# Kernel optimization log

Hardware: AMD Instinct MI355X
Metric: run time of the kernel (lower is better)

## Reference

```python
import jax, jax.numpy as jnp
import numpy as np

NH, HD = 8, 32  # num_heads, head_dim (visual_dim=256)
BASE = 10000.0

def _inv_freq(dim):
    return 1.0 / (BASE ** (jnp.arange(0, dim, 2, dtype=jnp.float32) / dim))

def rotate_half(x):
    x1, x2 = jnp.split(x, 2, axis=-1)
    return jnp.concatenate([-x2, x1], axis=-1)

def rope3d_freqs(D, H, W, head_dim):
    zd = head_dim // 3; yd = head_dim // 3; xd = head_dim - zd - yd
    fz = jnp.arange(D, dtype=jnp.float32)[:, None] * _inv_freq(zd)  # [D, zd/2]
    fy = jnp.arange(H, dtype=jnp.float32)[:, None] * _inv_freq(yd)
    fx = jnp.arange(W, dtype=jnp.float32)[:, None] * _inv_freq(xd)
    ez = jnp.broadcast_to(jnp.concatenate([fz, fz], -1)[:, None, None, :], (D, H, W, zd))
    ey = jnp.broadcast_to(jnp.concatenate([fy, fy], -1)[None, :, None, :], (D, H, W, yd))
    ex = jnp.broadcast_to(jnp.concatenate([fx, fx], -1)[None, None, :, :], (D, H, W, xd))
    return jnp.concatenate([ez, ey, ex], axis=-1)  # [D,H,W,head_dim]

def apply_rope(q, freqs):
    return q * jnp.cos(freqs) + rotate_half(q) * jnp.sin(freqs)

def setup_inputs() -> dict:
    key = jax.random.key(0)
    ks = jax.random.split(key, 16)
    B, C, D, H, W, S, TD = 2, 256, 32, 32, 32, 256, 512
    s = 0.02
    return {
        'fused_visual': jax.random.normal(ks[0], (B, C, D, H, W), jnp.float32),
        'text_embedding': jax.random.normal(ks[1], (B, S, TD), jnp.float32),
        'q_w': jax.random.normal(ks[2], (C, C), jnp.float32) * s,
        'q_b': jnp.zeros((C,), jnp.float32),
        'k_w': jax.random.normal(ks[3], (TD, C), jnp.float32) * s,
        'k_b': jnp.zeros((C,), jnp.float32),
        'v_w': jax.random.normal(ks[4], (TD, C), jnp.float32) * s,
        'v_b': jnp.zeros((C,), jnp.float32),
        'o_w': jax.random.normal(ks[5], (C, C), jnp.float32) * s,
        'o_b': jnp.zeros((C,), jnp.float32),
        'm1_w': jax.random.normal(ks[6], (TD, TD // 2), jnp.float32) * s,
        'm1_b': jnp.zeros((TD // 2,), jnp.float32),
        'm2_w': jax.random.normal(ks[7], (TD // 2, NH * HD), jnp.float32) * s,
        'm2_b': jnp.zeros((NH * HD,), jnp.float32),
    }

def reference(fused_visual, text_embedding, q_w, q_b, k_w, k_b, v_w, v_b,
              o_w, o_b, m1_w, m1_b, m2_w, m2_b):
    B, C, D, H, W = fused_visual.shape
    S = text_embedding.shape[1]
    scale = HD ** -0.5
    fv = jnp.transpose(fused_visual, (0, 2, 3, 4, 1))  # [B,D,H,W,C]
    q = (fv @ q_w + q_b).reshape(B, D, H, W, NH, HD)
    q = jnp.transpose(q, (0, 4, 1, 2, 3, 5))            # [B,nH,D,H,W,hd]
    k = jnp.transpose((text_embedding @ k_w + k_b).reshape(B, S, NH, HD), (0, 2, 1, 3))
    v = jnp.transpose((text_embedding @ v_w + v_b).reshape(B, S, NH, HD), (0, 2, 1, 3))
    freqs = rope3d_freqs(D, H, W, HD)[None, None]       # [1,1,D,H,W,hd]
    q_rot = apply_rope(q, freqs)
    # learned text phase (exact GELU as in torch default)
    h = jax.nn.gelu(text_embedding @ m1_w + m1_b, approximate=False)
    phase = jnp.transpose((h @ m2_w + m2_b).reshape(B, S, NH, HD), (0, 2, 1, 3))
    k_rot = apply_rope(k, phase)
    q_flat = q_rot.reshape(B, NH, D * H * W, HD)
    attn = jax.nn.softmax(jnp.einsum('bhnd,bhsd->bhns', q_flat, k_rot) * scale, axis=-1)
    out = jnp.einsum('bhns,bhsd->bhnd', attn, v)        # [B,nH,N,hd]
    out = out.reshape(B, NH, D, H, W, HD)
    out = jnp.transpose(out, (0, 2, 3, 4, 1, 5)).reshape(B, D, H, W, C)
    out = out @ o_w + o_b
    return jnp.transpose(out, (0, 4, 1, 2, 3))          # [B,C,D,H,W]
```

## Files before the change

### kernel.cpp

```cpp
#include <hip/hip_runtime.h>
#include <hip/hip_bf16.h>

#define NHD 8
#define HD  32
#define C_  256
#define TD_ 512
#define S_  256
#define N_  32768
#define B_  2

typedef short bf16x8 __attribute__((ext_vector_type(8)));
typedef short bf16x4 __attribute__((ext_vector_type(4)));
typedef float f32x4  __attribute__((ext_vector_type(4)));

#define MFMA16(a,b,c) __builtin_amdgcn_mfma_f32_16x16x32_bf16(a,b,c,0,0,0)

__device__ __forceinline__ short f2bf(float f){
    __hip_bfloat16 h = __float2bfloat16(f);
    return *reinterpret_cast<short*>(&h);
}

typedef __attribute__((address_space(3))) unsigned int lds_u32;
typedef const __attribute__((address_space(1))) unsigned int glb_u32;

__device__ __forceinline__ void async_cp16(const void* g, void* l){
    __builtin_amdgcn_global_load_lds(
        (glb_u32*)(unsigned long long)g,
        (lds_u32*)(unsigned int)(unsigned long long)l,
        16, 0, 0);
}

__device__ __forceinline__ void stage_tile(const short* __restrict__ g, short* l, int tid){
    const int wvb = tid & 192;
#pragma unroll
    for (int r = 0; r < 4; ++r)
        async_cp16(g + (r * 256 + tid) * 8, l + (r * 256 + wvb) * 8);
}

#define T1_LD(K,V,M,j0) _Pragma("unroll") for(int i=0;i<8;++i){ \
    K[i]=kp[(j0+i)*C_]; V[i]=vp[(j0+i)*C_]; M[i]=mp[(j0+i)*C_]; }
#define T1_FM(K,V,M,j0) _Pragma("unroll") for(int i=0;i<8;++i){ \
    _Pragma("unroll") for(int m=0;m<4;++m){ float tv=t_s[m*TD_+j0+i]; \
        accK[m]+=tv*K[i]; accV[m]+=tv*V[i]; accH[m]+=tv*M[i]; } }

__global__ __launch_bounds__(256) void text1(
    const float* __restrict__ text,
    const float* __restrict__ k_w, const float* __restrict__ k_b,
    const float* __restrict__ v_w, const float* __restrict__ v_b,
    const float* __restrict__ m1_w, const float* __restrict__ m1_b,
    const float* __restrict__ qw, const float* __restrict__ ow,
    float* __restrict__ kraw, float* __restrict__ vraw, float* __restrict__ hgb,
    short* __restrict__ wqf, short* __restrict__ wof)
{
    const int tid = threadIdx.x;

    if (blockIdx.x >= 128) {
        int gid = (blockIdx.x - 128) * 256 + tid;
        int m = gid >> 13;
        int rest = gid & 8191;
        const float* src = m ? ow : qw;
        short* dst = m ? wof : wqf;
        int lane = rest & 63;
        int l15 = lane & 15, qd = lane >> 4;
        int cbase, co;
        if (m == 0) { int nt = rest >> 9, cc = (rest >> 6) & 7; cbase = cc * 32 + qd * 8; co = nt * 16 + l15; }
        else        { int hm = rest >> 6; cbase = (hm >> 4) * 32 + qd * 8; co = (hm & 15) * 16 + l15; }
        bf16x8 r;
#pragma unroll
        for (int j = 0; j < 8; ++j) r[j] = f2bf(src[(size_t)(cbase + j) * 256 + co]);
        *(bf16x8*)&dst[(size_t)rest * 8] = r;
        return;
    }

    __shared__ float t_s[4 * TD_];
    const int tok0 = blockIdx.x * 4;
#pragma unroll
    for (int i = 0; i < 2; ++i) {
        int idx = i * 256 + tid;
        *(float4*)&t_s[idx * 4] = *(const float4*)&text[(size_t)tok0 * TD_ + idx * 4];
    }
    __syncthreads();

    float accK[4], accV[4], accH[4];
#pragma unroll
    for (int m = 0; m < 4; ++m) { accK[m] = k_b[tid]; accV[m] = v_b[tid]; accH[m] = m1_b[tid]; }
    const float* kp = k_w + tid;
    const float* vp = v_w + tid;
    const float* mp = m1_w + tid;

    {
        float ka[8], va[8], ma[8], kb2[8], vb2[8], mb2[8];
        T1_LD(ka, va, ma, 0);
#pragma unroll 1
        for (int j0 = 0; j0 < TD_; j0 += 16) {
            T1_LD(kb2, vb2, mb2, j0 + 8);
            T1_FM(ka, va, ma, j0);
            if (j0 + 16 < TD_) { T1_LD(ka, va, ma, j0 + 16); }
            T1_FM(kb2, vb2, mb2, j0 + 8);
        }
    }

#pragma unroll
    for (int m = 0; m < 4; ++m) {
        kraw[(size_t)(tok0 + m) * C_ + tid] = accK[m];
        vraw[(size_t)(tok0 + m) * C_ + tid] = accV[m];
        float hv = accH[m];
        hgb[(size_t)(tok0 + m) * C_ + tid] = 0.5f * hv * (1.0f + erff(hv * 0.70710678118654752f));
    }
}

#define T2_LD(G, j0) _Pragma("unroll") for (int i = 0; i < 8; ++i) G[i] = m2p[(j0 + i) * C_];
#define T2_FM(G, j0) _Pragma("unroll") for (int i = 0; i < 8; ++i) { \
    _Pragma("unroll") for (int m = 0; m < 8; ++m) accP[m] += h_s[m * C_ + j0 + i] * G[i]; }

__global__ __launch_bounds__(256) void text2(
    const float* __restrict__ m2_w, const float* __restrict__ m2_b,
    const float* __restrict__ kraw, const float* __restrict__ vraw,
    const float* __restrict__ hgb,
    short* __restrict__ kf, short* __restrict__ vf)
{
    __shared__ float h_s[8 * C_];
    const int tid = threadIdx.x;
    const int tok0 = blockIdx.x * 8;
#pragma unroll
    for (int i = 0; i < 2; ++i) {
        int idx = i * 256 + tid;
        *(float4*)&h_s[idx * 4] = *(const float4*)&hgb[(size_t)tok0 * C_ + idx * 4];
    }
    __syncthreads();

    float accP[8];
#pragma unroll
    for (int m = 0; m < 8; ++m) accP[m] = m2_b[tid];
    const float* m2p = m2_w + tid;
    {
        float ga[8], gb2[8];
        T2_LD(ga, 0);
#pragma unroll 1
        for (int j0 = 0; j0 < C_; j0 += 16) {
            T2_LD(gb2, j0 + 8);
            T2_FM(ga, j0);
            if (j0 + 16 < C_) { T2_LD(ga, j0 + 16); }
            T2_FM(gb2, j0 + 8);
        }
    }

    const int t = tid & (HD - 1);
    const int nh = tid >> 5;
#pragma unroll
    for (int m = 0; m < 8; ++m) {
        int token = tok0 + m;
        int b = token >> 8, s = token & (S_ - 1);
        int bh = b * NHD + nh;
        float kv = kraw[(size_t)token * C_ + tid];
        float vv = vraw[(size_t)token * C_ + tid];
        float partner = (t < 16) ? -kraw[(size_t)token * C_ + tid + 16]
                                 :  kraw[(size_t)token * C_ + tid - 16];
        float ph = accP[m];
        float kr = kv * cosf(ph) + partner * sinf(ph);
        kf[(((size_t)bh * 16 + (s >> 4)) * 64 + (t >> 3) * 16 + (s & 15)) * 8 + (t & 7)] = f2bf(kr);
        vf[((((size_t)bh * 8 + (s >> 5)) * 2 + (t >> 4)) * 64 + ((s >> 3) & 3) * 16 + (t & 15)) * 8 + (s & 7)] = f2bf(vv);
    }
}

__device__ __forceinline__ float freq3d(int t, int n){
    int d = n >> 10, h = (n >> 5) & 31, w = n & 31;
    float pos, ex;
    if (t < 10)      { pos = (float)d; ex = (float)(2 * (t % 5)) * 0.1f; }
    else if (t < 20) { pos = (float)h; ex = (float)(2 * ((t - 10) % 5)) * 0.1f; }
    else             { pos = (float)w; ex = (float)(2 * ((t - 20) % 6)) * (1.0f / 12.0f); }
    return pos * expf(-ex * 9.210340371976184f);
}

__global__ __launch_bounds__(256, 4) void fused_visual(
    const float* __restrict__ fv, const short* __restrict__ wqf,
    const float* __restrict__ q_b, const short* __restrict__ kf,
    const short* __restrict__ vf, const short* __restrict__ wof,
    const float* __restrict__ o_b, float* __restrict__ out)
{
    __shared__ __align__(16) short Stg[16384];
    __shared__ __align__(16) short Pb[4 * 16 * 64];
    const int tid = threadIdx.x;
    const int lane = tid & 63;
    const int l15 = tid & 15, qd = (tid >> 4) & 3, wv = tid >> 6;
    const int n0 = blockIdx.x * 64;
    const int b = blockIdx.y;
    const f32x4 z4 = {0.f, 0.f, 0.f, 0.f};
    const float scale = 0.17677669529663687f;

    short* slot0 = Stg;
    short* slot1 = Stg + 8192;

    stage_tile(wqf, slot0, tid);

    bf16x8 af[8];
    {
        const float* fbase = fv + ((size_t)b * C_) * N_ + n0 + wv * 16 + l15;
#pragma unroll
        for (int cc = 0; cc < 8; ++cc) {
            float tmp[8];
#pragma unroll
            for (int j = 0; j < 8; ++j)
                tmp[j] = fbase[(size_t)(cc * 32 + qd * 8 + j) * N_];
#pragma unroll
            for (int j = 0; j < 8; ++j) af[cc][j] = f2bf(tmp[j]);
        }
    }

    f32x4 acc[16];
#pragma unroll
    for (int i = 0; i < 16; ++i) acc[i] = z4;

#pragma unroll
    for (int ntp = 0; ntp < 8; ++ntp) {
        __syncthreads();
        if (ntp < 7) stage_tile(wqf + (ntp + 1) * 8192, (ntp & 1) ? slot0 : slot1, tid);
        const short* sb = (ntp & 1) ? slot1 : slot0;
#pragma unroll
        for (int cc = 0; cc < 8; ++cc)
#pragma unroll
            for (int ntl = 0; ntl < 2; ++ntl) {
                bf16x8 bq = *(const bf16x8*)&sb[((ntl * 8 + cc) * 64 + lane) * 8];
                acc[ntp * 2 + ntl] = MFMA16(af[cc], bq, acc[ntp * 2 + ntl]);
            }
    }
    __syncthreads();

    short* Qsc = Stg + wv * 4096;
#pragma unroll
    for (int r = 0; r < 4; ++r) {
        int lr = qd * 4 + r;
        int n = n0 + wv * 16 + lr;
        int key = lr & 7;
        float f1 = freq3d(l15, n), f2 = freq3d(l15 + 16, n);
        float c1 = cosf(f1), s1 = sinf(f1), c2 = cosf(f2), s2 = sinf(f2);
#pragma unroll
        for (int hh = 0; hh < 8; ++hh) {
            float x1 = acc[2 * hh][r]     + q_b[hh * 32 + l15];
            float x2 = acc[2 * hh + 1][r] + q_b[hh * 32 + 16 + l15];
            int cb1 = (hh * 4 + (l15 >> 3)) ^ key;
            int cb2 = (hh * 4 + 2 + (l15 >> 3)) ^ key;
            Qsc[lr * 256 + cb1 * 8 + (l15 & 7)] = f2bf((x1 * c1 - x2 * s1) * scale);
            Qsc[lr * 256 + cb2 * 8 + (l15 & 7)] = f2bf((x2 * c2 + x1 * s2) * scale);
        }
    }
    bf16x8 aqh[8];
#pragma unroll
    for (int h = 0; h < 8; ++h)
        aqh[h] = *(const bf16x8*)&Qsc[l15 * 256 + ((h * 4 + qd) ^ (l15 & 7)) * 8];

    __syncthreads();
    stage_tile(kf + (size_t)(b * NHD) * 8192, slot0, tid);

    f32x4 acc_co[16];
#pragma unroll
    for (int i = 0; i < 16; ++i) acc_co[i] = z4;
    short* Pw = Pb + wv * 16 * 64;
    short* Ow = Pw;

#pragma unroll
    for (int h = 0; h < 8; ++h) {
        const int bh = b * NHD + h;
        __syncthreads();
        stage_tile(wof + (size_t)h * 8192, slot1, tid);

        const short* vbase = vf + (size_t)bh * 8192;

        float tsum[4] = {0.f, 0.f, 0.f, 0.f};
        f32x4 o0 = z4, o1 = z4;

#pragma unroll
        for (int qt = 0; qt < 4; ++qt) {
            f32x4 sc[4];
#pragma unroll
            for (int s4 = 0; s4 < 4; ++s4) {
                bf16x8 bk = *(const bf16x8*)&slot0[(qt * 4 + s4) * 512 + lane * 8];
                sc[s4] = MFMA16(aqh[h], bk, z4);
            }
#pragma unroll
            for (int s4 = 0; s4 < 4; ++s4)
#pragma unroll
                for (int r = 0; r < 4; ++r) {
                    sc[s4][r] = __expf(sc[s4][r]);
                    tsum[r] += sc[s4][r];
                }
#pragma unroll
            for (int s4 = 0; s4 < 4; ++s4)
#pragma unroll
                for (int r = 0; r < 4; ++r) {
                    int row = qd * 4 + r;
                    Pw[row * 64 + ((s4 * 2 + (l15 >> 3)) ^ (row & 7)) * 8 + (l15 & 7)] = f2bf(sc[s4][r]);
                }
#pragma unroll
            for (int ktl = 0; ktl < 2; ++ktl) {
                bf16x8 pa = *(const bf16x8*)&Pw[l15 * 64 + ((ktl * 4 + qd) ^ (l15 & 7)) * 8];
                int kt = qt * 2 + ktl;
                bf16x8 v0 = *(const bf16x8*)&vbase[(kt * 2 + 0) * 512 + lane * 8];
                bf16x8 v1 = *(const bf16x8*)&vbase[(kt * 2 + 1) * 512 + lane * 8];
                o0 = MFMA16(pa, v0, o0);
                o1 = MFMA16(pa, v1, o1);
            }
        }
        float il[4];
#pragma unroll
        for (int r = 0; r < 4; ++r) {
            float t = tsum[r];
            t += __shfl_xor(t, 1); t += __shfl_xor(t, 2);
            t += __shfl_xor(t, 4); t += __shfl_xor(t, 8);
            il[r] = 1.f / t;
        }
#pragma unroll
        for (int r = 0; r < 4; ++r) {
            int row = qd * 4 + r;
            int key = row & 3;
            Ow[row * 32 + (((l15 >> 3) ^ key) & 3) * 8 + (l15 & 7)]       = f2bf(o0[r] * il[r]);
            Ow[row * 32 + (((2 + (l15 >> 3)) ^ key) & 3) * 8 + (l15 & 7)] = f2bf(o1[r] * il[r]);
        }

        __syncthreads();
        if (h < 7)
            stage_tile(kf + (size_t)(bh + 1) * 8192, slot0, tid);

        bf16x8 bo = *(const bf16x8*)&Ow[l15 * 32 + ((qd ^ (l15 & 3)) & 3) * 8];
#pragma unroll
        for (int mt = 0; mt < 16; ++mt) {
            bf16x8 ao = *(const bf16x8*)&slot1[mt * 512 + lane * 8];
            acc_co[mt] = MFMA16(ao, bo, acc_co[mt]);
        }
    }

#pragma unroll
    for (int mt = 0; mt < 16; ++mt)
#pragma unroll
        for (int r = 0; r < 4; ++r) {
            int co = mt * 16 + qd * 4 + r;
            out[(size_t)(b * C_ + co) * N_ + n0 + wv * 16 + l15] = acc_co[mt][r] + o_b[co];
        }
}

extern "C" void kernel_launch(void* const* d_in, const int* in_sizes, int n_in,
                              void* d_out, int out_size, void* d_ws, size_t ws_size,
                              hipStream_t stream) {
    (void)in_sizes; (void)n_in; (void)out_size; (void)ws_size;
    const float* fv   = (const float*)d_in[0];
    const float* text = (const float*)d_in[1];
    const float* q_w  = (const float*)d_in[2];
    const float* q_b  = (const float*)d_in[3];
    const float* k_w  = (const float*)d_in[4];
    const float* k_b  = (const float*)d_in[5];
    const float* v_w  = (const float*)d_in[6];
    const float* v_b  = (const float*)d_in[7];
    const float* o_w  = (const float*)d_in[8];
    const float* o_b  = (const float*)d_in[9];
    const float* m1_w = (const float*)d_in[10];
    const float* m1_b = (const float*)d_in[11];
    const float* m2_w = (const float*)d_in[12];
    const float* m2_b = (const float*)d_in[13];
    float* out = (float*)d_out;

    short* wsS  = (short*)d_ws;
    short* kf   = wsS;
    short* vf   = wsS + 131072;
    short* wqf  = wsS + 262144;
    short* wof  = wsS + 327680;
    float* kraw = (float*)(wsS + 393216);
    float* vraw = kraw + 131072;
    float* hgb  = kraw + 262144;

    hipLaunchKernelGGL(text1, dim3(192), dim3(256), 0, stream,
                       text, k_w, k_b, v_w, v_b, m1_w, m1_b,
                       q_w, o_w, kraw, vraw, hgb, wqf, wof);
    hipLaunchKernelGGL(text2, dim3(64), dim3(256), 0, stream,
                       m2_w, m2_b, kraw, vraw, hgb, kf, vf);
    hipLaunchKernelGGL(fused_visual, dim3(512, 2), dim3(256), 0, stream,
                       fv, wqf, q_b, kf, vf, wof, o_b, out);
}
```

Baseline: 309.0 us.

## Fuse text kernels into one and stage visual input via async LDS copies

Merges the two text-side kernels into a single kernel that keeps K, V and the GELU hidden state in shared memory instead of writing raw intermediates to global memory, which removes one launch and a global round trip. In the fused visual kernel, the strided per-thread fp32 loads of the input tile are replaced by coalesced async global-to-LDS copies with an XOR swizzle, double-buffered over four channel quarters, before conversion to bf16 fragments. The Q weight tile staging is moved after this input load. Extra LDS use and added barriers may cut occupancy or add sync cost.

```diff
diff --git a/kernel.cpp b/kernel.cpp
--- a/kernel.cpp
+++ b/kernel.cpp
@@ -42,14 +42,18 @@
 #define T1_FM(K,V,M,j0) _Pragma("unroll") for(int i=0;i<8;++i){ \
     _Pragma("unroll") for(int m=0;m<4;++m){ float tv=t_s[m*TD_+j0+i]; \
         accK[m]+=tv*K[i]; accV[m]+=tv*V[i]; accH[m]+=tv*M[i]; } }
-
-__global__ __launch_bounds__(256) void text1(
+#define T2_LD(G, j0) _Pragma("unroll") for (int i = 0; i < 8; ++i) G[i] = m2p[(j0 + i) * C_];
+#define T2_FM(G, j0) _Pragma("unroll") for (int i = 0; i < 8; ++i) { \
+    _Pragma("unroll") for (int m = 0; m < 4; ++m) accP[m] += h_s[m * C_ + j0 + i] * G[i]; }
+
+__global__ __launch_bounds__(256) void text_all(
     const float* __restrict__ text,
     const float* __restrict__ k_w, const float* __restrict__ k_b,
     const float* __restrict__ v_w, const float* __restrict__ v_b,
     const float* __restrict__ m1_w, const float* __restrict__ m1_b,
+    const float* __restrict__ m2_w, const float* __restrict__ m2_b,
     const float* __restrict__ qw, const float* __restrict__ ow,
-    float* __restrict__ kraw, float* __restrict__ vraw, float* __restrict__ hgb,
+    short* __restrict__ kf, short* __restrict__ vf,
     short* __restrict__ wqf, short* __restrict__ wof)
 {
     const int tid = threadIdx.x;
@@ -73,6 +77,8 @@
     }
 
     __shared__ float t_s[4 * TD_];
+    __shared__ float h_s[4 * C_];
+    __shared__ float k_s[4 * C_];
     const int tok0 = blockIdx.x * 4;
 #pragma unroll
     for (int i = 0; i < 2; ++i) {
@@ -102,36 +108,15 @@
 
 #pragma unroll
     for (int m = 0; m < 4; ++m) {
-        kraw[(size_t)(tok0 + m) * C_ + tid] = accK[m];
-        vraw[(size_t)(tok0 + m) * C_ + tid] = accV[m];
+        k_s[m * C_ + tid] = accK[m];
         float hv = accH[m];
-        hgb[(size_t)(tok0 + m) * C_ + tid] = 0.5f * hv * (1.0f + erff(hv * 0.70710678118654752f));
-    }
-}
-
-#define T2_LD(G, j0) _Pragma("unroll") for (int i = 0; i < 8; ++i) G[i] = m2p[(j0 + i) * C_];
-#define T2_FM(G, j0) _Pragma("unroll") for (int i = 0; i < 8; ++i) { \
-    _Pragma("unroll") for (int m = 0; m < 8; ++m) accP[m] += h_s[m * C_ + j0 + i] * G[i]; }
-
-__global__ __launch_bounds__(256) void text2(
-    const float* __restrict__ m2_w, const float* __restrict__ m2_b,
-    const float* __restrict__ kraw, const float* __restrict__ vraw,
-    const float* __restrict__ hgb,
-    short* __restrict__ kf, short* __restrict__ vf)
-{
-    __shared__ float h_s[8 * C_];
-    const int tid = threadIdx.x;
-    const int tok0 = blockIdx.x * 8;
-#pragma unroll
-    for (int i = 0; i < 2; ++i) {
-        int idx = i * 256 + tid;
-        *(float4*)&h_s[idx * 4] = *(const float4*)&hgb[(size_t)tok0 * C_ + idx * 4];
+        h_s[m * C_ + tid] = 0.5f * hv * (1.0f + erff(hv * 0.70710678118654752f));
     }
     __syncthreads();
 
-    float accP[8];
-#pragma unroll
-    for (int m = 0; m < 8; ++m) accP[m] = m2_b[tid];
+    float accP[4];
+#pragma unroll
+    for (int m = 0; m < 4; ++m) accP[m] = m2_b[tid];
     const float* m2p = m2_w + tid;
     {
         float ga[8], gb2[8];
@@ -148,14 +133,13 @@
     const int t = tid & (HD - 1);
     const int nh = tid >> 5;
 #pragma unroll
-    for (int m = 0; m < 8; ++m) {
+    for (int m = 0; m < 4; ++m) {
         int token = tok0 + m;
         int b = token >> 8, s = token & (S_ - 1);
         int bh = b * NHD + nh;
-        float kv = kraw[(size_t)token * C_ + tid];
-        float vv = vraw[(size_t)token * C_ + tid];
-        float partner = (t < 16) ? -kraw[(size_t)token * C_ + tid + 16]
-                                 :  kraw[(size_t)token * C_ + tid - 16];
+        float kv = k_s[m * C_ + tid];
+        float vv = accV[m];
+        float partner = (t < 16) ? -k_s[m * C_ + tid + 16] : k_s[m * C_ + tid - 16];
         float ph = accP[m];
         float kr = kv * cosf(ph) + partner * sinf(ph);
         kf[(((size_t)bh * 16 + (s >> 4)) * 64 + (t >> 3) * 16 + (s & 15)) * 8 + (t & 7)] = f2bf(kr);
@@ -191,25 +175,54 @@
     short* slot0 = Stg;
     short* slot1 = Stg + 8192;
 
-    stage_tile(wqf, slot0, tid);
-
     bf16x8 af[8];
     {
-        const float* fbase = fv + ((size_t)b * C_) * N_ + n0 + wv * 16 + l15;
-#pragma unroll
-        for (int cc = 0; cc < 8; ++cc) {
-            float tmp[8];
-#pragma unroll
-            for (int j = 0; j < 8; ++j)
-                tmp[j] = fbase[(size_t)(cc * 32 + qd * 8 + j) * N_];
-#pragma unroll
-            for (int j = 0; j < 8; ++j) af[cc][j] = f2bf(tmp[j]);
-        }
+        const float* fvb = fv + (size_t)(b * C_) * N_ + n0;
+        auto stage_q = [&](int qq, short* s) {
+#pragma unroll
+            for (int r = 0; r < 4; ++r) {
+                int slot = r * 256 + tid;
+                int c_loc = slot >> 4;
+                int key = ((c_loc >> 3) << 1) & 15;
+                int u = (slot & 15) ^ key;
+                async_cp16(fvb + (size_t)(qq * 64 + c_loc) * N_ + u * 4,
+                           s + (r * 256 + (tid & 192)) * 8);
+            }
+        };
+        auto gather_q = [&](int qq, const short* s) {
+            const float* Tsf = (const float*)s;
+#pragma unroll
+            for (int cc2 = 0; cc2 < 2; ++cc2) {
+                bf16x8 a;
+#pragma unroll
+                for (int j = 0; j < 8; ++j) {
+                    int c_loc = cc2 * 32 + qd * 8 + j;
+                    int key = ((c_loc >> 3) << 1) & 15;
+                    int pos = (wv * 4 + (l15 >> 2)) ^ key;
+                    a[j] = f2bf(Tsf[c_loc * 64 + pos * 4 + (l15 & 3)]);
+                }
+                af[qq * 2 + cc2] = a;
+            }
+        };
+        stage_q(0, slot0);
+        stage_q(1, slot1);
+        __syncthreads();
+        gather_q(0, slot0);
+        __syncthreads();
+        stage_q(2, slot0);
+        gather_q(1, slot1);
+        __syncthreads();
+        stage_q(3, slot1);
+        gather_q(2, slot0);
+        __syncthreads();
+        gather_q(3, slot1);
     }
 
     f32x4 acc[16];
 #pragma unroll
     for (int i = 0; i < 16; ++i) acc[i] = z4;
+
+    stage_tile(wqf, slot0, tid);
 
 #pragma unroll
     for (int ntp = 0; ntp < 8; ++ntp) {
@@ -363,15 +376,10 @@
     short* vf   = wsS + 131072;
     short* wqf  = wsS + 262144;
     short* wof  = wsS + 327680;
-    float* kraw = (float*)(wsS + 393216);
-    float* vraw = kraw + 131072;
-    float* hgb  = kraw + 262144;
-
-    hipLaunchKernelGGL(text1, dim3(192), dim3(256), 0, stream,
-                       text, k_w, k_b, v_w, v_b, m1_w, m1_b,
-                       q_w, o_w, kraw, vraw, hgb, wqf, wof);
-    hipLaunchKernelGGL(text2, dim3(64), dim3(256), 0, stream,
-                       m2_w, m2_b, kraw, vraw, hgb, kf, vf);
+
+    hipLaunchKernelGGL(text_all, dim3(192), dim3(256), 0, stream,
+                       text, k_w, k_b, v_w, v_b, m1_w, m1_b, m2_w, m2_b,
+                       q_w, o_w, kf, vf, wqf, wof);
     hipLaunchKernelGGL(fused_visual, dim3(512, 2), dim3(256), 0, stream,
                        fv, wqf, q_b, kf, vf, wof, o_b, out);
 }
```

Result: no change. 305.2 us (-1.2%).
